# Optimization experiments

Hardware: AMD Instinct MI355X
Metric: run time of the kernel (lower is better)

## Reference

```python
import jax, jax.numpy as jnp
import numpy as np


def setup_inputs() -> dict:
    key = jax.random.key(0)
    k1, k2 = jax.random.split(key)
    x1 = jax.random.normal(k1, (8192, 64), dtype=jnp.float32)
    x2 = jax.random.normal(k2, (8192, 64), dtype=jnp.float32)
    return {"x1": x1, "x2": x2}


def reference(x1, x2):
    # squared Euclidean distance: ||a-b||^2 = ||a||^2 + ||b||^2 - 2 a.b
    sq1 = jnp.sum(x1 * x1, axis=-1, keepdims=True)        # [N, 1]
    sq2 = jnp.sum(x2 * x2, axis=-1, keepdims=True).T      # [1, M]
    cross = jnp.einsum('nd,md->nm', x1, x2)               # [N, M] GEMM
    d2 = sq1 + sq2 - 2.0 * cross
    # clamp tiny negatives from floating-point cancellation (cdist>=0)
    return jnp.maximum(d2, 0.0)
```

## Files before the change

kernel.cpp:

```cpp
#include <hip/hip_runtime.h>


typedef __bf16 bf16x8 __attribute__((ext_vector_type(8)));
typedef float floatx4 __attribute__((ext_vector_type(4)));
typedef unsigned short ushort8 __attribute__((ext_vector_type(8)));

#define TILE 128
#define KD 64
#define LDSS 72

__device__ __forceinline__ unsigned short f2bf(float x) {
    union { float f; unsigned int u; } v; v.f = x;
    return (unsigned short)((v.u + 0x7FFFu + ((v.u >> 16) & 1u)) >> 16);
}

__global__ void sqeuclid_mfma(const float* __restrict__ x1,
                              const float* __restrict__ x2,
                              float* __restrict__ out,
                              int M) {
    __shared__ unsigned short a_s[TILE][LDSS];
    __shared__ unsigned short b_s[TILE][LDSS];
    __shared__ float sq1_s[TILE];
    __shared__ float sq2_s[TILE];

    const int t = threadIdx.x;
    const int block_row = blockIdx.y * TILE;
    const int block_col = blockIdx.x * TILE;

    {
        const int r = t & 127;
        const float* src = (t < TILE) ? (x1 + (size_t)(block_row + r) * KD)
                                      : (x2 + (size_t)(block_col + r) * KD);
        unsigned short* dst = (t < TILE) ? a_s[r] : b_s[r];
        float nrm = 0.f;
        #pragma unroll
        for (int i = 0; i < 8; ++i) {
            const float4 f0 = ((const float4*)src)[2 * i];
            const float4 f1 = ((const float4*)src)[2 * i + 1];
            nrm = fmaf(f0.x, f0.x, nrm); nrm = fmaf(f0.y, f0.y, nrm);
            nrm = fmaf(f0.z, f0.z, nrm); nrm = fmaf(f0.w, f0.w, nrm);
            nrm = fmaf(f1.x, f1.x, nrm); nrm = fmaf(f1.y, f1.y, nrm);
            nrm = fmaf(f1.z, f1.z, nrm); nrm = fmaf(f1.w, f1.w, nrm);
            ushort8 pk;
            pk[0] = f2bf(f0.x); pk[1] = f2bf(f0.y); pk[2] = f2bf(f0.z); pk[3] = f2bf(f0.w);
            pk[4] = f2bf(f1.x); pk[5] = f2bf(f1.y); pk[6] = f2bf(f1.z); pk[7] = f2bf(f1.w);
            *(ushort8*)&dst[i * 8] = pk;
        }
        if (t < TILE) sq1_s[r] = nrm; else sq2_s[r] = nrm;
    }
    __syncthreads();

    const int wave = t >> 6, lane = t & 63;
    const int wr = (wave >> 1) * 64;
    const int wc = (wave & 1) * 64;
    const int lm = lane & 15, lq = lane >> 4;

    floatx4 acc[4][4];
    #pragma unroll
    for (int i = 0; i < 4; ++i)
        #pragma unroll
        for (int j = 0; j < 4; ++j)
            acc[i][j] = (floatx4){0.f, 0.f, 0.f, 0.f};

    #pragma unroll
    for (int ks = 0; ks < 2; ++ks) {
        const int koff = ks * 32 + lq * 8;
        bf16x8 afr[4], bfr[4];
        #pragma unroll
        for (int i = 0; i < 4; ++i) {
            afr[i] = *(const bf16x8*)&a_s[wr + i * 16 + lm][koff];
            bfr[i] = *(const bf16x8*)&b_s[wc + i * 16 + lm][koff];
        }
        #pragma unroll
        for (int i = 0; i < 4; ++i)
            #pragma unroll
            for (int j = 0; j < 4; ++j)
                acc[i][j] = __builtin_amdgcn_mfma_f32_16x16x32_bf16(
                    bfr[i], afr[j], acc[i][j], 0, 0, 0);
    }

    floatx4 s2q[4];
    #pragma unroll
    for (int i = 0; i < 4; ++i)
        s2q[i] = *(const floatx4*)&sq2_s[wc + i * 16 + lq * 4];

    #pragma unroll
    for (int j = 0; j < 4; ++j) {
        const int lrow = wr + j * 16 + lm;
        const float s1 = sq1_s[lrow];
        const size_t gbase = (size_t)(block_row + lrow) * M + block_col;
        #pragma unroll
        for (int i = 0; i < 4; ++i) {
            const int lcol = wc + i * 16 + lq * 4;
            floatx4 v;
            #pragma unroll
            for (int r = 0; r < 4; ++r)
                v[r] = fmaxf(fmaf(-2.f, acc[i][j][r], s1 + s2q[i][r]), 0.f);
            __builtin_nontemporal_store(v, (floatx4*)(out + gbase + lcol));
        }
    }
}

extern "C" void kernel_launch(void* const* d_in, const int* in_sizes, int n_in,
                              void* d_out, int out_size, void* d_ws, size_t ws_size,
                              hipStream_t stream) {
    const float* x1 = (const float*)d_in[0];
    const float* x2 = (const float*)d_in[1];
    float* out = (float*)d_out;
    const int N = in_sizes[0] / KD;
    const int M = in_sizes[1] / KD;

    dim3 grid(M / TILE, N / TILE);
    dim3 block(256);
    sqeuclid_mfma<<<grid, block, 0, stream>>>(x1, x2, out, M);
}
```

Baseline: 296.5 us.

## Precompute bf16 rows and norms once in workspace, then GEMM from global

```diff
diff --git a/kernel.cpp b/kernel.cpp
--- a/kernel.cpp
+++ b/kernel.cpp
@@ -14,10 +14,101 @@
     return (unsigned short)((v.u + 0x7FFFu + ((v.u >> 16) & 1u)) >> 16);
 }
 
-__global__ void sqeuclid_mfma(const float* __restrict__ x1,
-                              const float* __restrict__ x2,
-                              float* __restrict__ out,
-                              int M) {
+__global__ __launch_bounds__(256) void convert_rows(
+        const float* __restrict__ x1,
+        const float* __restrict__ x2,
+        unsigned short* __restrict__ xb1,
+        unsigned short* __restrict__ xb2,
+        float* __restrict__ sq1,
+        float* __restrict__ sq2,
+        int N, int M) {
+    const int tid = blockIdx.x * blockDim.x + threadIdx.x;
+    if (tid >= N + M) return;
+    const int r = (tid < N) ? tid : tid - N;
+    const float* src = (tid < N) ? (x1 + (size_t)r * KD) : (x2 + (size_t)r * KD);
+    unsigned short* dst = (tid < N) ? (xb1 + (size_t)r * KD) : (xb2 + (size_t)r * KD);
+    float nrm = 0.f;
+    #pragma unroll
+    for (int i = 0; i < 8; ++i) {
+        const float4 f0 = ((const float4*)src)[2 * i];
+        const float4 f1 = ((const float4*)src)[2 * i + 1];
+        nrm = fmaf(f0.x, f0.x, nrm); nrm = fmaf(f0.y, f0.y, nrm);
+        nrm = fmaf(f0.z, f0.z, nrm); nrm = fmaf(f0.w, f0.w, nrm);
+        nrm = fmaf(f1.x, f1.x, nrm); nrm = fmaf(f1.y, f1.y, nrm);
+        nrm = fmaf(f1.z, f1.z, nrm); nrm = fmaf(f1.w, f1.w, nrm);
+        ushort8 pk;
+        pk[0] = f2bf(f0.x); pk[1] = f2bf(f0.y); pk[2] = f2bf(f0.z); pk[3] = f2bf(f0.w);
+        pk[4] = f2bf(f1.x); pk[5] = f2bf(f1.y); pk[6] = f2bf(f1.z); pk[7] = f2bf(f1.w);
+        *(ushort8*)&dst[i * 8] = pk;
+    }
+    if (tid < N) sq1[r] = nrm; else sq2[r] = nrm;
+}
+
+__global__ __launch_bounds__(256) void sqeuclid_main(
+        const unsigned short* __restrict__ xb1,
+        const unsigned short* __restrict__ xb2,
+        const float* __restrict__ sq1,
+        const float* __restrict__ sq2,
+        float* __restrict__ out, int M) {
+    const int t = threadIdx.x;
+    const int block_row = blockIdx.y * TILE;
+    const int block_col = blockIdx.x * TILE;
+    const int wave = t >> 6, lane = t & 63;
+    const int wr = (wave >> 1) * 64;
+    const int wc = (wave & 1) * 64;
+    const int lm = lane & 15, lq = lane >> 4;
+
+    const int arow = block_row + wr + lm;
+    const int brow = block_col + wc + lm;
+
+    floatx4 acc[4][4];
+    #pragma unroll
+    for (int i = 0; i < 4; ++i)
+        #pragma unroll
+        for (int j = 0; j < 4; ++j)
+            acc[i][j] = (floatx4){0.f, 0.f, 0.f, 0.f};
+
+    #pragma unroll
+    for (int ks = 0; ks < 2; ++ks) {
+        const int koff = ks * 32 + lq * 8;
+        bf16x8 afr[4], bfr[4];
+        #pragma unroll
+        for (int i = 0; i < 4; ++i) {
+            afr[i] = *(const bf16x8*)&xb1[(size_t)(arow + i * 16) * KD + koff];
+            bfr[i] = *(const bf16x8*)&xb2[(size_t)(brow + i * 16) * KD + koff];
+        }
+        #pragma unroll
+        for (int i = 0; i < 4; ++i)
+            #pragma unroll
+            for (int j = 0; j < 4; ++j)
+                acc[i][j] = __builtin_amdgcn_mfma_f32_16x16x32_bf16(
+                    bfr[i], afr[j], acc[i][j], 0, 0, 0);
+    }
+
+    floatx4 s2q[4];
+    #pragma unroll
+    for (int i = 0; i < 4; ++i)
+        s2q[i] = *(const floatx4*)&sq2[block_col + wc + i * 16 + lq * 4];
+
+    #pragma unroll
+    for (int j = 0; j < 4; ++j) {
+        const int lrow = wr + j * 16 + lm;
+        const float s1 = sq1[block_row + lrow];
+        const size_t gbase = (size_t)(block_row + lrow) * M + block_col;
+        #pragma unroll
+        for (int i = 0; i < 4; ++i) {
+            floatx4 v;
+            #pragma unroll
+            for (int r = 0; r < 4; ++r)
+                v[r] = fmaxf(fmaf(-2.f, acc[i][j][r], s1 + s2q[i][r]), 0.f);
+            *(floatx4*)(out + gbase + wc + i * 16 + lq * 4) = v;
+        }
+    }
+}
+
+__global__ void sqeuclid_fused(const float* __restrict__ x1,
+                               const float* __restrict__ x2,
+                               float* __restrict__ out, int M) {
     __shared__ unsigned short a_s[TILE][LDSS];
     __shared__ unsigned short b_s[TILE][LDSS];
     __shared__ float sq1_s[TILE];
@@ -26,7 +117,6 @@
     const int t = threadIdx.x;
     const int block_row = blockIdx.y * TILE;
     const int block_col = blockIdx.x * TILE;
-
     {
         const int r = t & 127;
         const float* src = (t < TILE) ? (x1 + (size_t)(block_row + r) * KD)
@@ -91,12 +181,11 @@
         const size_t gbase = (size_t)(block_row + lrow) * M + block_col;
         #pragma unroll
         for (int i = 0; i < 4; ++i) {
-            const int lcol = wc + i * 16 + lq * 4;
             floatx4 v;
             #pragma unroll
             for (int r = 0; r < 4; ++r)
                 v[r] = fmaxf(fmaf(-2.f, acc[i][j][r], s1 + s2q[i][r]), 0.f);
-            __builtin_nontemporal_store(v, (floatx4*)(out + gbase + lcol));
+            *(floatx4*)(out + gbase + wc + i * 16 + lq * 4) = v;
         }
     }
 }
@@ -112,5 +201,23 @@
 
     dim3 grid(M / TILE, N / TILE);
     dim3 block(256);
-    sqeuclid_mfma<<<grid, block, 0, stream>>>(x1, x2, out, M);
-}
+
+    const size_t xb1_off = 0;
+    const size_t xb2_off = (size_t)N * KD * 2;
+    const size_t sq1_off = xb2_off + (size_t)M * KD * 2;
+    const size_t sq2_off = sq1_off + (size_t)N * 4;
+    const size_t ws_needed = sq2_off + (size_t)M * 4;
+
+    if (d_ws != nullptr && ws_size >= ws_needed) {
+        unsigned short* xb1 = (unsigned short*)((char*)d_ws + xb1_off);
+        unsigned short* xb2 = (unsigned short*)((char*)d_ws + xb2_off);
+        float* sq1 = (float*)((char*)d_ws + sq1_off);
+        float* sq2 = (float*)((char*)d_ws + sq2_off);
+        const int rows = N + M;
+        convert_rows<<<dim3((rows + 255) / 256), dim3(256), 0, stream>>>(
+            x1, x2, xb1, xb2, sq1, sq2, N, M);
+        sqeuclid_main<<<grid, block, 0, stream>>>(xb1, xb2, sq1, sq2, out, M);
+    } else {
+        sqeuclid_fused<<<grid, block, 0, stream>>>(x1, x2, out, M);
+    }
+}
```

Measured after the change: 274.4 us (median of 2 runs). -7.5%, faster.
